# Kernel optimization log

Hardware: AMD Instinct MI355X
Metric: run time of the kernel (lower is better)

Reference implementation:

```python
import math
import jax, jax.numpy as jnp
import numpy as np

# fixed model constants (ToyConfig / UTParams defaults)
DT = 0.05; CDAMP = 0.25; AP = 0.1; AV = 0.1; JIT = 1e-6
N = 4; NY = 2
ALPHA = 0.8; BETA = 2.0; KAPPA = 0.0
LAM = ALPHA ** 2 * (N + KAPPA) - N
CUT = N + LAM
SQRT_C = math.sqrt(CUT)
_wm = np.full(2 * N + 1, 1.0 / (2.0 * CUT), dtype=np.float32); _wm[0] = LAM / CUT
_wc = _wm.copy(); _wc[0] = LAM / CUT + (1.0 - ALPHA ** 2 + BETA)
WM = jnp.asarray(_wm); WC = jnp.asarray(_wc)
Q = jnp.diag(jnp.array([1e-5, 1e-4, 1e-6, 1e-6], dtype=jnp.float32))
R = jnp.diag(jnp.array([0.05 ** 2, 0.05 ** 2], dtype=jnp.float32))

B = 16384; T = 256


def _sym(A):
    return 0.5 * (A + A.swapaxes(-1, -2))


def _chol(A):
    # safe_cholesky: symmetrize + jitter*I (first try always succeeds here)
    n = A.shape[-1]
    return jnp.linalg.cholesky(_sym(A) + JIT * jnp.eye(n, dtype=A.dtype))


def _sigma_points(mean, cov):
    # mean (B,n), cov (B,n,n) -> (B,2n+1,n)
    L = _chol(cov)
    A = SQRT_C * L.swapaxes(-1, -2)  # rows are sigma offsets
    m = mean[:, None, :]
    return jnp.concatenate([m, m + A, m - A], axis=1)


def _f_duffing(z, u):
    # z (B,S,4), u (B,1)
    p, v, k, al = z[..., 0], z[..., 1], z[..., 2], z[..., 3]
    p2 = p + DT * v
    v2 = v + DT * (-CDAMP * v - k * p - al * p ** 3 + u)
    return jnp.stack([p2, v2, k, al], axis=-1)


def _h(z):
    p, v = z[..., 0], z[..., 1]
    return jnp.stack([p + AP * p ** 3, v + AV * v ** 3], axis=-1)


def _kalman_gain(P_zy, S):
    # K = P_zy S^{-1} via cholesky solve
    L = _chol(S)
    Y = jax.scipy.linalg.solve_triangular(L, P_zy.swapaxes(-1, -2), lower=True)
    K_T = jax.scipy.linalg.solve_triangular(L.swapaxes(-1, -2), Y, lower=False)
    return K_T.swapaxes(-1, -2)


def _update(z_pred, P_pred, X_sigma, y_t):
    Y = _h(X_sigma)                                   # (B,9,2)
    y_pred = jnp.einsum('bsi,s->bi', Y, WM)
    dY = Y - y_pred[:, None, :]
    dX = X_sigma - z_pred[:, None, :]
    S = jnp.einsum('bsi,bsj,s->bij', dY, dY, WC) + R
    S = _sym(S) + JIT * jnp.eye(NY, dtype=S.dtype)
    P_zy = jnp.einsum('bsi,bsj,s->bij', dX, dY, WC)
    nu = y_t - y_pred
    K = _kalman_gain(P_zy, S)
    z_post = z_pred + jnp.einsum('bij,bj->bi', K, nu)
    # generalized Joseph update
    P_post = (P_pred - K @ P_zy.swapaxes(-1, -2) - P_zy @ K.swapaxes(-1, -2)
              + K @ S @ K.swapaxes(-1, -2))
    P_post = _sym(P_post) + JIT * jnp.eye(N, dtype=P_post.dtype)
    return z_post, P_post


def _ukf(y, u, z0, P0):
    # t = 0: no dynamics, sigma points of prior directly
    sig0 = _sigma_points(z0, P0)
    z, P = _update(z0, P0, sig0, y[:, 0, :])

    def body(carry, inputs):
        z, P = carry
        y_t, u_prev = inputs                           # (B,2), (B,)
        sig = _sigma_points(z, P)
        Xs = _f_duffing(sig, u_prev[:, None])
        z_pred = jnp.einsum('bsi,s->bi', Xs, WM)
        dX = Xs - z_pred[:, None, :]
        P_pred = jnp.einsum('bsi,bsj,s->bij', dX, dX, WC) + Q
        P_pred = _sym(P_pred) + JIT * jnp.eye(N, dtype=P_pred.dtype)
        z_post, P_post = _update(z_pred, P_pred, Xs, y_t)
        return (z_post, P_post), z_post

    ys = jnp.swapaxes(y[:, 1:, :], 0, 1)               # (T-1,B,2)
    us = jnp.swapaxes(u[:, : y.shape[1] - 1], 0, 1)    # u_prev = u[:, t-1]
    (_, _), z_rest = jax.lax.scan(body, (z, P), (ys, us))
    z_hist = jnp.concatenate([z[:, None, :], jnp.swapaxes(z_rest, 0, 1)], axis=1)
    return z_hist                                      # (B,T,4)


def setup_inputs() -> dict:
    key = jax.random.key(0)
    k1, k2, k3, k4 = jax.random.split(key, 4)
    y = jax.random.normal(k1, (B, T, NY), dtype=jnp.float32)
    u = jax.random.normal(k2, (B, T), dtype=jnp.float32)
    z0 = 0.1 * jax.random.normal(k3, (B, N), dtype=jnp.float32) + jnp.array([1.0, 0.0, 1.0, 0.4], dtype=jnp.float32)
    A = 0.05 * jax.random.normal(k4, (B, N, N), dtype=jnp.float32)
    P0 = 0.1 * jnp.eye(N, dtype=jnp.float32) + A @ A.swapaxes(-1, -2)  # SPD
    return {"y": y, "u": u, "z0": z0, "P0": P0}


def reference(y, u, z0, P0):
    return _ukf(y, u, z0, P0)
```

## Files before the change

### kernel.cpp

```cpp
#include <hip/hip_runtime.h>
#include <math.h>

#ifndef __has_builtin
#define __has_builtin(x) 0
#endif

__device__ __forceinline__ float fsqrt(float x){
#if __has_builtin(__builtin_amdgcn_sqrtf)
    return __builtin_amdgcn_sqrtf(x);
#else
    return sqrtf(x);
#endif
}
__device__ __forceinline__ float frsqrt(float x){
#if __has_builtin(__builtin_amdgcn_rsqf)
    return __builtin_amdgcn_rsqf(x);
#else
    return 1.0f/sqrtf(x);
#endif
}
__device__ __forceinline__ float frcp(float x){
#if __has_builtin(__builtin_amdgcn_rcpf)
    return __builtin_amdgcn_rcpf(x);
#else
    return 1.0f/x;
#endif
}

namespace {
constexpr int TT = 256;
constexpr int BB = 16384;
}

__global__ __launch_bounds__(64)
void ukf_kernel(const float* __restrict__ yg, const float* __restrict__ ug,
                const float* __restrict__ z0g, const float* __restrict__ P0g,
                float* __restrict__ outg)
{
    constexpr float DT  = 0.05f, CD = 0.25f, AP = 0.1f, AV = 0.1f;
    constexpr float CJ  = 2.56e-6f;
    constexpr float CVV = 1.0f - DT*CD;
    constexpr float WM0 = -0.5625f, WC0 = 1.7975f;
    constexpr float W2  = 0.390625f;
    constexpr float WA  = 2.57875f;
    constexpr float WAC = 6.6016f;
    constexpr float WCC = 4.6016f;
    constexpr float W2E = 0.1171875f;
    constexpr float RSG = 0.00640512f;
    constexpr float CQ2C = 1.53125f;
    constexpr float CB00 = 3.072e-5f;
    constexpr float CB11 = 2.6112e-4f;
    constexpr float CB22 = 1.024e-5f;
    constexpr float HCUT = 1.28f;
    constexpr float CUTc = 2.56f;

    const int b = blockIdx.x*64 + threadIdx.x;

    float z0v = z0g[b*4+0], z1v = z0g[b*4+1], z2v = z0g[b*4+2], z3v = z0g[b*4+3];
    const float* Pb = P0g + (size_t)b*16;
    float P00 = CUTc*Pb[0];
    float P01 = HCUT*(Pb[1]+Pb[4]);
    float P02 = HCUT*(Pb[2]+Pb[8]);
    float P03 = HCUT*(Pb[3]+Pb[12]);
    float P11 = CUTc*Pb[5];
    float P12 = HCUT*(Pb[6]+Pb[9]);
    float P13 = HCUT*(Pb[7]+Pb[13]);
    float P22 = CUTc*Pb[10];
    float P23 = HCUT*(Pb[11]+Pb[14]);
    float P33 = CUTc*Pb[15];

    const float* yb = yg + (size_t)b*TT*2;
    const float* ub = ug + (size_t)b*TT;
    float*       ob = outg + (size_t)b*TT*4;

    float g00,g10,g20,g30,g11,g21,g31,g22,g32,g33;

    auto chol = [&](){
        float a00 = P00 + CJ;
        float r0  = frsqrt(a00);
        g00 = a00*r0;
        g10 = P01*r0;
        g20 = P02*r0;
        g30 = P03*r0;
        float a11 = fmaf(-g10,g10, P11 + CJ);
        float r1  = frsqrt(a11);
        g11 = a11*r1;
        g21 = fmaf(-g20,g10, P12)*r1;
        g31 = fmaf(-g30,g10, P13)*r1;
        float a22 = fmaf(-g21,g21, fmaf(-g20,g20, P22 + CJ));
        float r2  = frsqrt(a22);
        g22 = a22*r2;
        g32 = fmaf(-g31,g21, fmaf(-g30,g20, P23))*r2;
        float a33 = fmaf(-g32,g32, fmaf(-g31,g31, fmaf(-g30,g30, P33 + CJ)));
        g33 = fsqrt(a33);
    };

    auto update = [&](float X00, float X01, float Xp, float Xm,
                      float D10, float q,
                      float D00, float D01, float D11, float D12, float D13,
                      float B00p,float B01p,float B02p,float B03p,float B11p,
                      float B12p,float B13p,float B22p,float B23p,float B33p,
                      float yv0, float yv1)
    {
        float eps_c = -W2*q;
        float eps_a = q + eps_c;
        float zp1   = fmaf(W2, q, X01);

        float w0 = X00*X00, w1 = X01*X01;
        float apx = AP*X00, avx = AV*X01;
        float Y00 = fmaf(apx, w0, X00);
        float Y01 = fmaf(avx, w1, X01);
        float cp  = fmaf(0.3f, w0, 1.0f);
        float cv  = fmaf(0.3f, w1, 1.0f);
        float e3p = 0.3f*X00, e3v = 0.3f*X01;
        float w2e3p = W2E*X00;

        float D00sq = D00*D00, D01sq = D01*D01;
        float SD0 = D00sq + D01sq;
        float yp0 = fmaf(w2e3p, SD0, Y00);
        float ec0 = Y00 - yp0;
        float xi0 = fmaf(e3p, D00sq, ec0);
        float xi1 = fmaf(e3p, D01sq, ec0);
        float Od00 = D00*fmaf(AP, D00sq, cp);
        float Od01 = D01*fmaf(AP, D01sq, cp);

        float sp = Xp*Xp, sm = Xm*Xm;
        float Yp = fmaf(AV*Xp, sp, Xp);
        float Ym = fmaf(AV*Xm, sm, Xm);
        float qy = fmaf(0.5f, Yp + Ym, -Y01);
        float Q0 = 0.5f*(Yp - Ym);

        float D11sq = D11*D11, D12sq = D12*D12, D13sq = D13*D13;
        float SD1 = (D11sq + D12sq) + D13sq;
        float inner = fmaf(e3v, SD1, qy);
        float yp1 = fmaf(W2, inner, Y01);
        float ec1 = Y01 - yp1;
        float et0 = qy + ec1;
        float et1 = fmaf(e3v, D11sq, ec1);
        float et2 = fmaf(e3v, D12sq, ec1);
        float et3 = fmaf(e3v, D13sq, ec1);
        float Q1 = D11*fmaf(AV, D11sq, cv);
        float Q2 = D12*fmaf(AV, D12sq, cv);
        float Q3 = D13*fmaf(AV, D13sq, cv);
        float et23 = et2 + et3;

        float Ts00 = fmaf(Od00,Od00, xi0*xi0);
        Ts00 = fmaf(xi1,xi1,Ts00); Ts00 = fmaf(Od01,Od01,Ts00);
        float s00 = fmaf(WAC, ec0*ec0, Ts00);
        float Ts01 = fmaf(Od00, Q0, xi0*et0);
        Ts01 = fmaf(xi1, et1, Ts01); Ts01 = fmaf(Od01, Q1, Ts01);
        Ts01 = fmaf(ec0, et23, Ts01);
        float s01 = fmaf(WCC, ec0*ec1, Ts01);
        float Ts11 = fmaf(Q0,Q0, et0*et0);
        Ts11 = fmaf(et1,et1,Ts11); Ts11 = fmaf(Q1,Q1,Ts11);
        Ts11 = fmaf(et2,et2,Ts11); Ts11 = fmaf(Q2,Q2,Ts11);
        Ts11 = fmaf(et3,et3,Ts11); Ts11 = fmaf(Q3,Q3,Ts11);
        float s11 = fmaf(WCC, ec1*ec1, Ts11);

        float pz00 = fmaf(D01, Od01, D00*Od00);
        float pz01 = fmaf(D01, Q1, D00*Q0);
        float Tp10 = fmaf(D10, Od00, eps_a*xi0);
        Tp10 = fmaf(eps_c, xi1, Tp10); Tp10 = fmaf(D11, Od01, Tp10);
        float pz10 = fmaf(-WA, q*ec0, Tp10);
        float et123 = et1 + et23;
        float Tp11 = fmaf(D10, Q0, eps_a*et0);
        Tp11 = fmaf(eps_c, et123, Tp11);
        Tp11 = fmaf(D11, Q1, Tp11);
        Tp11 = fmaf(D12, Q2, Tp11);
        Tp11 = fmaf(D13, Q3, Tp11);
        float pz11 = fmaf(-WC0, q*ec1, Tp11);
        float pz20 = fmaf(g21, Od01, g20*Od00);
        float pz30 = fmaf(g31, Od01, g30*Od00);
        float pz21 = fmaf(g21, Q1, g20*Q0); pz21 = fmaf(g22, Q2, pz21);
        float pz31 = fmaf(g31, Q1, g30*Q0); pz31 = fmaf(g32, Q2, pz31);
        pz31 = fmaf(g33, Q3, pz31);

        float sg00 = s00 + RSG, sg11 = s11 + RSG;
        float det  = fmaf(sg00, sg11, -(s01*s01));
        float idet = frcp(det);
        float i00 = sg11*idet, i01 = -(s01*idet), i11 = sg00*idet;
        float K00 = fmaf(pz01,i01, pz00*i00), K01 = fmaf(pz01,i11, pz00*i01);
        float K10 = fmaf(pz11,i01, pz10*i00), K11 = fmaf(pz11,i11, pz10*i01);
        float K20 = fmaf(pz21,i01, pz20*i00), K21 = fmaf(pz21,i11, pz20*i01);
        float K30 = fmaf(pz31,i01, pz30*i00), K31 = fmaf(pz31,i11, pz30*i01);

        float nu0 = yv0 - yp0, nu1 = yv1 - yp1;
        z0v = fmaf(K00,nu0, fmaf(K01,nu1, X00));
        z1v = fmaf(K10,nu0, fmaf(K11,nu1, zp1));
        z2v = fmaf(K20,nu0, fmaf(K21,nu1, z2v));
        z3v = fmaf(K30,nu0, fmaf(K31,nu1, z3v));

        P00 = fmaf(-K00,pz00, fmaf(-K01,pz01, B00p));
        P01 = fmaf(-K00,pz10, fmaf(-K01,pz11, B01p));
        P02 = fmaf(-K00,pz20, fmaf(-K01,pz21, B02p));
        P03 = fmaf(-K00,pz30, fmaf(-K01,pz31, B03p));
        P11 = fmaf(-K10,pz10, fmaf(-K11,pz11, B11p));
        P12 = fmaf(-K10,pz20, fmaf(-K11,pz21, B12p));
        P13 = fmaf(-K10,pz30, fmaf(-K11,pz31, B13p));
        P22 = fmaf(-K20,pz20, fmaf(-K21,pz21, B22p));
        P23 = fmaf(-K20,pz30, fmaf(-K21,pz31, B23p));
        P33 = fmaf(-K30,pz30, fmaf(-K31,pz31, B33p));
    };

    float2 ycur  = *reinterpret_cast<const float2*>(yb);
    float2 ynext = *reinterpret_cast<const float2*>(yb + 2);
    float  unext = ub[0];

    chol();
    update(z0v, z1v, z1v+g10, z1v-g10,
           g10, 0.0f,
           g00, 0.0f, g11, 0.0f, 0.0f,
           P00+CJ, P01, P02, P03, P11+CJ, P12, P13, P22+CJ, P23, P33+CJ,
           ycur.x, ycur.y);
    *reinterpret_cast<float4*>(ob) = make_float4(z0v, z1v, z2v, z3v);

    #pragma unroll 1
    for (int t = 1; t < TT; ++t) {
        float yv0 = ynext.x, yv1 = ynext.y;
        float uu  = unext;
        int tn = (t+1 < TT) ? (t+1) : (TT-1);
        ynext = *reinterpret_cast<const float2*>(yb + 2*tn);
        unext = ub[t];

        chol();

        float w  = z0v*z0v;
        float zc = w*z0v;
        float X00 = fmaf(DT, z1v, z0v);
        float ac = fmaf(-CD, z1v, uu);
        ac = fmaf(-z2v, z0v, ac);
        ac = fmaf(-z3v, zc, ac);
        float X01 = fmaf(DT, ac, z1v);

        float pp = z0v+g00, pm = z0v-g00;
        float vp = z1v+g10, vm = z1v-g10;
        float kp = z2v+g20, km = z2v-g20;
        float aap = z3v+g30, aam = z3v-g30;
        float cp3 = (pp*pp)*pp, cm3 = (pm*pm)*pm;
        float accp = fmaf(-CD, vp, uu); accp = fmaf(-kp,pp,accp); accp = fmaf(-aap,cp3,accp);
        float Xp = fmaf(DT, accp, vp);
        float accm = fmaf(-CD, vm, uu); accm = fmaf(-km,pm,accm); accm = fmaf(-aam,cm3,accm);
        float Xm = fmaf(DT, accm, vm);
        float D10 = 0.5f*(Xp - Xm);
        float q   = fmaf(0.5f, Xp + Xm, -X01);

        float D00 = fmaf(DT, g10, g00);
        float D01 = DT*g11;
        float ha  = fmaf(g31, zc, g21*z0v);
        float D11 = fmaf(CVV, g11, -(DT*ha));
        float hb  = fmaf(g32, zc, g22*z0v);
        float D12 = -(DT*hb);
        float D13 = -(DT*(g33*zc));

        float B00p = fmaf(D01,D01, fmaf(D00,D00, CB00));
        float B01p = fmaf(D01, D11, D00*D10);
        float B02p = fmaf(D01, g21, D00*g20);
        float B03p = fmaf(D01, g31, D00*g30);
        float TB11 = fmaf(D10,D10, CB11);
        TB11 = fmaf(D11,D11,TB11); TB11 = fmaf(D12,D12,TB11); TB11 = fmaf(D13,D13,TB11);
        float B11p = fmaf(CQ2C, q*q, TB11);
        float B12p = fmaf(D11,g21, D10*g20); B12p = fmaf(D12,g22,B12p);
        float B13p = fmaf(D11,g31, D10*g30); B13p = fmaf(D12,g32,B13p);
        B13p = fmaf(D13,g33,B13p);
        float B22p = P22 + CB22;
        float B23p = P23;
        float B33p = P33 + CB22;

        update(X00, X01, Xp, Xm, D10, q, D00, D01, D11, D12, D13,
               B00p,B01p,B02p,B03p,B11p,B12p,B13p,B22p,B23p,B33p, yv0, yv1);

        *reinterpret_cast<float4*>(ob + 4*t) = make_float4(z0v, z1v, z2v, z3v);
    }
}

extern "C" void kernel_launch(void* const* d_in, const int* in_sizes, int n_in,
                              void* d_out, int out_size, void* d_ws, size_t ws_size,
                              hipStream_t stream) {
    const float* y  = (const float*)d_in[0];
    const float* u  = (const float*)d_in[1];
    const float* z0 = (const float*)d_in[2];
    const float* P0 = (const float*)d_in[3];
    float* out = (float*)d_out;

    ukf_kernel<<<dim3(BB/64), dim3(64), 0, stream>>>(y, u, z0, P0, out);
}
```

Before: 129.6 us.

## Process two independent filter chains per thread to expose instruction-level parallelism

```diff
diff --git a/kernel.cpp b/kernel.cpp
--- a/kernel.cpp
+++ b/kernel.cpp
@@ -30,52 +30,54 @@
 namespace {
 constexpr int TT = 256;
 constexpr int BB = 16384;
-}
-
-__global__ __launch_bounds__(64)
-void ukf_kernel(const float* __restrict__ yg, const float* __restrict__ ug,
-                const float* __restrict__ z0g, const float* __restrict__ P0g,
-                float* __restrict__ outg)
-{
-    constexpr float DT  = 0.05f, CD = 0.25f, AP = 0.1f, AV = 0.1f;
-    constexpr float CJ  = 2.56e-6f;
-    constexpr float CVV = 1.0f - DT*CD;
-    constexpr float WM0 = -0.5625f, WC0 = 1.7975f;
-    constexpr float W2  = 0.390625f;
-    constexpr float WA  = 2.57875f;
-    constexpr float WAC = 6.6016f;
-    constexpr float WCC = 4.6016f;
-    constexpr float W2E = 0.1171875f;
-    constexpr float RSG = 0.00640512f;
-    constexpr float CQ2C = 1.53125f;
-    constexpr float CB00 = 3.072e-5f;
-    constexpr float CB11 = 2.6112e-4f;
-    constexpr float CB22 = 1.024e-5f;
-    constexpr float HCUT = 1.28f;
-    constexpr float CUTc = 2.56f;
-
-    const int b = blockIdx.x*64 + threadIdx.x;
-
-    float z0v = z0g[b*4+0], z1v = z0g[b*4+1], z2v = z0g[b*4+2], z3v = z0g[b*4+3];
-    const float* Pb = P0g + (size_t)b*16;
-    float P00 = CUTc*Pb[0];
-    float P01 = HCUT*(Pb[1]+Pb[4]);
-    float P02 = HCUT*(Pb[2]+Pb[8]);
-    float P03 = HCUT*(Pb[3]+Pb[12]);
-    float P11 = CUTc*Pb[5];
-    float P12 = HCUT*(Pb[6]+Pb[9]);
-    float P13 = HCUT*(Pb[7]+Pb[13]);
-    float P22 = CUTc*Pb[10];
-    float P23 = HCUT*(Pb[11]+Pb[14]);
-    float P33 = CUTc*Pb[15];
-
-    const float* yb = yg + (size_t)b*TT*2;
-    const float* ub = ug + (size_t)b*TT;
-    float*       ob = outg + (size_t)b*TT*4;
-
+constexpr float DT  = 0.05f, CD = 0.25f, AP = 0.1f, AV = 0.1f;
+constexpr float CJ  = 2.56e-6f;
+constexpr float CVV = 1.0f - DT*CD;
+constexpr float WM0 = -0.5625f, WC0 = 1.7975f;
+constexpr float W2  = 0.390625f;
+constexpr float WA  = 2.57875f;
+constexpr float WAC = 6.6016f;
+constexpr float WCC = 4.6016f;
+constexpr float W2E = 0.1171875f;
+constexpr float RSG = 0.00640512f;
+constexpr float CQ2C = 1.53125f;
+constexpr float CB00 = 3.072e-5f;
+constexpr float CB11 = 2.6112e-4f;
+constexpr float CB22 = 1.024e-5f;
+constexpr float HCUT = 1.28f;
+constexpr float CUTc = 2.56f;
+}
+
+struct UKF {
+    float z0v,z1v,z2v,z3v;
+    float P00,P01,P02,P03,P11,P12,P13,P22,P23,P33;
     float g00,g10,g20,g30,g11,g21,g31,g22,g32,g33;
-
-    auto chol = [&](){
+    float X00,X01,Xp,Xm,D10,q,D00,D01,D11,D12,D13;
+    float B00p,B01p,B02p,B03p,B11p,B12p,B13p,B22p,B23p,B33p;
+    const float *yb, *ub; float *ob;
+    float2 ynext; float unext;
+
+    __device__ __forceinline__ void load(const float* yg, const float* ug,
+                                         const float* z0g, const float* P0g,
+                                         float* outg, int b){
+        z0v=z0g[b*4+0]; z1v=z0g[b*4+1]; z2v=z0g[b*4+2]; z3v=z0g[b*4+3];
+        const float* Pb = P0g + (size_t)b*16;
+        P00 = CUTc*Pb[0];
+        P01 = HCUT*(Pb[1]+Pb[4]);
+        P02 = HCUT*(Pb[2]+Pb[8]);
+        P03 = HCUT*(Pb[3]+Pb[12]);
+        P11 = CUTc*Pb[5];
+        P12 = HCUT*(Pb[6]+Pb[9]);
+        P13 = HCUT*(Pb[7]+Pb[13]);
+        P22 = CUTc*Pb[10];
+        P23 = HCUT*(Pb[11]+Pb[14]);
+        P33 = CUTc*Pb[15];
+        yb = yg + (size_t)b*TT*2;
+        ub = ug + (size_t)b*TT;
+        ob = outg + (size_t)b*TT*4;
+    }
+
+    __device__ __forceinline__ void chol(){
         float a00 = P00 + CJ;
         float r0  = frsqrt(a00);
         g00 = a00*r0;
@@ -93,15 +95,61 @@
         g32 = fmaf(-g31,g21, fmaf(-g30,g20, P23))*r2;
         float a33 = fmaf(-g32,g32, fmaf(-g31,g31, fmaf(-g30,g30, P33 + CJ)));
         g33 = fsqrt(a33);
-    };
-
-    auto update = [&](float X00, float X01, float Xp, float Xm,
-                      float D10, float q,
-                      float D00, float D01, float D11, float D12, float D13,
-                      float B00p,float B01p,float B02p,float B03p,float B11p,
-                      float B12p,float B13p,float B22p,float B23p,float B33p,
-                      float yv0, float yv1)
-    {
+    }
+
+    __device__ __forceinline__ void predict0(){
+        X00=z0v; X01=z1v; Xp=z1v+g10; Xm=z1v-g10;
+        D10=g10; q=0.0f; D00=g00; D01=0.0f; D11=g11; D12=0.0f; D13=0.0f;
+        B00p=P00+CJ; B01p=P01; B02p=P02; B03p=P03;
+        B11p=P11+CJ; B12p=P12; B13p=P13;
+        B22p=P22+CJ; B23p=P23; B33p=P33+CJ;
+    }
+
+    __device__ __forceinline__ void predict(float uu){
+        float w  = z0v*z0v;
+        float zc = w*z0v;
+        X00 = fmaf(DT, z1v, z0v);
+        float ac = fmaf(-CD, z1v, uu);
+        ac = fmaf(-z2v, z0v, ac);
+        ac = fmaf(-z3v, zc, ac);
+        X01 = fmaf(DT, ac, z1v);
+
+        float pp = z0v+g00, pm = z0v-g00;
+        float vp = z1v+g10, vm = z1v-g10;
+        float kp = z2v+g20, km = z2v-g20;
+        float aap = z3v+g30, aam = z3v-g30;
+        float cp3 = (pp*pp)*pp, cm3 = (pm*pm)*pm;
+        float accp = fmaf(-CD, vp, uu); accp = fmaf(-kp,pp,accp); accp = fmaf(-aap,cp3,accp);
+        Xp = fmaf(DT, accp, vp);
+        float accm = fmaf(-CD, vm, uu); accm = fmaf(-km,pm,accm); accm = fmaf(-aam,cm3,accm);
+        Xm = fmaf(DT, accm, vm);
+        D10 = 0.5f*(Xp - Xm);
+        q   = fmaf(0.5f, Xp + Xm, -X01);
+
+        D00 = fmaf(DT, g10, g00);
+        D01 = DT*g11;
+        float ha  = fmaf(g31, zc, g21*z0v);
+        D11 = fmaf(CVV, g11, -(DT*ha));
+        float hb  = fmaf(g32, zc, g22*z0v);
+        D12 = -(DT*hb);
+        D13 = -(DT*(g33*zc));
+
+        B00p = fmaf(D01,D01, fmaf(D00,D00, CB00));
+        B01p = fmaf(D01, D11, D00*D10);
+        B02p = fmaf(D01, g21, D00*g20);
+        B03p = fmaf(D01, g31, D00*g30);
+        float TB11 = fmaf(D10,D10, CB11);
+        TB11 = fmaf(D11,D11,TB11); TB11 = fmaf(D12,D12,TB11); TB11 = fmaf(D13,D13,TB11);
+        B11p = fmaf(CQ2C, q*q, TB11);
+        B12p = fmaf(D11,g21, D10*g20); B12p = fmaf(D12,g22,B12p);
+        B13p = fmaf(D11,g31, D10*g30); B13p = fmaf(D12,g32,B13p);
+        B13p = fmaf(D13,g33,B13p);
+        B22p = P22 + CB22;
+        B23p = P23;
+        B33p = P33 + CB22;
+    }
+
+    __device__ __forceinline__ void update(float yv0, float yv1){
         float eps_c = -W2*q;
         float eps_a = q + eps_c;
         float zp1   = fmaf(W2, q, X01);
@@ -200,76 +248,50 @@
         P22 = fmaf(-K20,pz20, fmaf(-K21,pz21, B22p));
         P23 = fmaf(-K20,pz30, fmaf(-K21,pz31, B23p));
         P33 = fmaf(-K30,pz30, fmaf(-K31,pz31, B33p));
-    };
-
-    float2 ycur  = *reinterpret_cast<const float2*>(yb);
-    float2 ynext = *reinterpret_cast<const float2*>(yb + 2);
-    float  unext = ub[0];
-
-    chol();
-    update(z0v, z1v, z1v+g10, z1v-g10,
-           g10, 0.0f,
-           g00, 0.0f, g11, 0.0f, 0.0f,
-           P00+CJ, P01, P02, P03, P11+CJ, P12, P13, P22+CJ, P23, P33+CJ,
-           ycur.x, ycur.y);
-    *reinterpret_cast<float4*>(ob) = make_float4(z0v, z1v, z2v, z3v);
+    }
+
+    __device__ __forceinline__ void store(int t){
+        *reinterpret_cast<float4*>(ob + 4*t) = make_float4(z0v,z1v,z2v,z3v);
+    }
+};
+
+__global__ __launch_bounds__(64)
+void ukf_kernel(const float* __restrict__ yg, const float* __restrict__ ug,
+                const float* __restrict__ z0g, const float* __restrict__ P0g,
+                float* __restrict__ outg)
+{
+    const int tid = blockIdx.x*64 + threadIdx.x;
+
+    UKF A, B;
+    A.load(yg,ug,z0g,P0g,outg, tid);
+    B.load(yg,ug,z0g,P0g,outg, tid + BB/2);
+
+    float2 ayc = *reinterpret_cast<const float2*>(A.yb);
+    float2 byc = *reinterpret_cast<const float2*>(B.yb);
+    A.ynext = *reinterpret_cast<const float2*>(A.yb + 2);
+    B.ynext = *reinterpret_cast<const float2*>(B.yb + 2);
+    A.unext = A.ub[0];
+    B.unext = B.ub[0];
+
+    A.chol();               B.chol();
+    A.predict0();           B.predict0();
+    A.update(ayc.x, ayc.y); B.update(byc.x, byc.y);
+    A.store(0);             B.store(0);
 
     #pragma unroll 1
     for (int t = 1; t < TT; ++t) {
-        float yv0 = ynext.x, yv1 = ynext.y;
-        float uu  = unext;
+        float ay0=A.ynext.x, ay1=A.ynext.y, au=A.unext;
+        float by0=B.ynext.x, by1=B.ynext.y, bu=B.unext;
         int tn = (t+1 < TT) ? (t+1) : (TT-1);
-        ynext = *reinterpret_cast<const float2*>(yb + 2*tn);
-        unext = ub[t];
-
-        chol();
-
-        float w  = z0v*z0v;
-        float zc = w*z0v;
-        float X00 = fmaf(DT, z1v, z0v);
-        float ac = fmaf(-CD, z1v, uu);
-        ac = fmaf(-z2v, z0v, ac);
-        ac = fmaf(-z3v, zc, ac);
-        float X01 = fmaf(DT, ac, z1v);
-
-        float pp = z0v+g00, pm = z0v-g00;
-        float vp = z1v+g10, vm = z1v-g10;
-        float kp = z2v+g20, km = z2v-g20;
-        float aap = z3v+g30, aam = z3v-g30;
-        float cp3 = (pp*pp)*pp, cm3 = (pm*pm)*pm;
-        float accp = fmaf(-CD, vp, uu); accp = fmaf(-kp,pp,accp); accp = fmaf(-aap,cp3,accp);
-        float Xp = fmaf(DT, accp, vp);
-        float accm = fmaf(-CD, vm, uu); accm = fmaf(-km,pm,accm); accm = fmaf(-aam,cm3,accm);
-        float Xm = fmaf(DT, accm, vm);
-        float D10 = 0.5f*(Xp - Xm);
-        float q   = fmaf(0.5f, Xp + Xm, -X01);
-
-        float D00 = fmaf(DT, g10, g00);
-        float D01 = DT*g11;
-        float ha  = fmaf(g31, zc, g21*z0v);
-        float D11 = fmaf(CVV, g11, -(DT*ha));
-        float hb  = fmaf(g32, zc, g22*z0v);
-        float D12 = -(DT*hb);
-        float D13 = -(DT*(g33*zc));
-
-        float B00p = fmaf(D01,D01, fmaf(D00,D00, CB00));
-        float B01p = fmaf(D01, D11, D00*D10);
-        float B02p = fmaf(D01, g21, D00*g20);
-        float B03p = fmaf(D01, g31, D00*g30);
-        float TB11 = fmaf(D10,D10, CB11);
-        TB11 = fmaf(D11,D11,TB11); TB11 = fmaf(D12,D12,TB11); TB11 = fmaf(D13,D13,TB11);
-        float B11p = fmaf(CQ2C, q*q, TB11);
-        float B12p = fmaf(D11,g21, D10*g20); B12p = fmaf(D12,g22,B12p);
-        float B13p = fmaf(D11,g31, D10*g30); B13p = fmaf(D12,g32,B13p);
-        B13p = fmaf(D13,g33,B13p);
-        float B22p = P22 + CB22;
-        float B23p = P23;
-        float B33p = P33 + CB22;
-
-        update(X00, X01, Xp, Xm, D10, q, D00, D01, D11, D12, D13,
-               B00p,B01p,B02p,B03p,B11p,B12p,B13p,B22p,B23p,B33p, yv0, yv1);
-
-        *reinterpret_cast<float4*>(ob + 4*t) = make_float4(z0v, z1v, z2v, z3v);
+        A.ynext = *reinterpret_cast<const float2*>(A.yb + 2*tn);
+        B.ynext = *reinterpret_cast<const float2*>(B.yb + 2*tn);
+        A.unext = A.ub[t];
+        B.unext = B.ub[t];
+
+        A.chol();            B.chol();
+        A.predict(au);       B.predict(bu);
+        A.update(ay0, ay1);  B.update(by0, by1);
+        A.store(t);          B.store(t);
     }
 }
 
@@ -282,5 +304,5 @@
     const float* P0 = (const float*)d_in[3];
     float* out = (float*)d_out;
 
-    ukf_kernel<<<dim3(BB/64), dim3(64), 0, stream>>>(y, u, z0, P0, out);
-}
+    ukf_kernel<<<dim3((BB/2)/64), dim3(64), 0, stream>>>(y, u, z0, P0, out);
+}
```

Result: slower. 264.9 us (+104.4%).
